# Optimization experiments

Hardware: AMD Instinct MI355X
Metric: run time of the kernel (lower is better)

Reference implementation:

```python
import jax, jax.numpy as jnp
import numpy as np
from jax import lax

B, L, V = 128, 64, 8192
E = H = 128
STEPS = 10
MAX_BIN = 512
BETA_START, BETA_END = 1e-4, 2e-2


def setup_inputs():
    key = jax.random.key(0)
    k = jax.random.split(key, 23)
    s = 0.05
    padded_x = (jax.random.uniform(k[0], (B, L, V)) < 0.01).astype(jnp.float32)
    lengths = jax.random.randint(k[1], (B,), 1, L + 1)
    visit_mask = (jnp.arange(L)[None, :] < lengths[:, None]).astype(jnp.float32)
    padded_bins = jnp.sort(jax.random.randint(k[2], (B, L), 0, MAX_BIN), axis=1)
    t_diff = jax.random.randint(k[3], (B,), 1, STEPS + 1)
    eps = jax.random.normal(k[4], (B, L, E))
    z0 = jax.random.normal(k[5], (B, L, E))
    noise = jax.random.normal(k[6], (STEPS, B, L, E))
    W_visit = jax.random.normal(k[7], (E, V)) * s
    bin_embed = (jax.random.normal(k[8], (MAX_BIN + 2, E)) * s).at[0].set(0.0)  # padding_idx=0
    W_ih = jax.random.normal(k[9], (4 * H, E)) * s
    W_hh = jax.random.normal(k[10], (4 * H, H)) * s
    b_ih = jax.random.normal(k[11], (4 * H,)) * s
    b_hh = jax.random.normal(k[12], (4 * H,)) * s
    W_cls = jax.random.normal(k[13], (1, H)) * s
    b_cls = jax.random.normal(k[14], (1,)) * s
    W_proj = jax.random.normal(k[15], (E, H)) * s
    time_embed = jax.random.normal(k[16], (STEPS + 1, E)) * s
    W_fuse = jax.random.normal(k[17], (2, 2 * E)) * s
    b_fuse = jax.random.normal(k[18], (2,)) * s
    W_e1 = jax.random.normal(k[19], (E, 2 * E)) * s
    b_e1 = jax.random.normal(k[20], (E,)) * s
    W_e2 = jax.random.normal(k[21], (E, E)) * s
    b_e2 = jax.random.normal(k[22], (E,)) * s
    return dict(padded_x=padded_x, visit_mask=visit_mask, padded_bins=padded_bins,
                t_diff=t_diff, eps=eps, z0=z0, noise=noise, W_visit=W_visit,
                bin_embed=bin_embed, W_ih=W_ih, W_hh=W_hh, b_ih=b_ih, b_hh=b_hh,
                W_cls=W_cls, b_cls=b_cls, W_proj=W_proj, time_embed=time_embed,
                W_fuse=W_fuse, b_fuse=b_fuse, W_e1=W_e1, b_e1=b_e1, W_e2=W_e2, b_e2=b_e2)


def _lstm(v, W_ih, W_hh, b_ih, b_hh):
    # v: [B,L,E] -> h: [B,L,H]; PyTorch gate order i,f,g,o
    xg = jnp.einsum('ble,ge->blg', v, W_ih) + b_ih + b_hh
    def step(carry, x):
        h, c = carry
        g = x + h @ W_hh.T
        i, f, gg, o = jnp.split(g, 4, axis=-1)
        c = jax.nn.sigmoid(f) * c + jax.nn.sigmoid(i) * jnp.tanh(gg)
        h = jax.nn.sigmoid(o) * jnp.tanh(c)
        return (h, c), h
    z = jnp.zeros((v.shape[0], W_hh.shape[1]), v.dtype)
    _, hs = lax.scan(step, (z, z), jnp.swapaxes(xg, 0, 1))
    return jnp.swapaxes(hs, 0, 1)


def _last_hidden(h, mask):
    lengths = jnp.maximum(mask.sum(axis=1).astype(jnp.int32), 1)
    return h[jnp.arange(h.shape[0]), lengths - 1]


def reference(padded_x, visit_mask, padded_bins, t_diff, eps, z0, noise,
              W_visit, bin_embed, W_ih, W_hh, b_ih, b_hh, W_cls, b_cls,
              W_proj, time_embed, W_fuse, b_fuse, W_e1, b_e1, W_e2, b_e2):
    m = visit_mask[..., None]                      # [B,L,1]
    betas = jnp.linspace(BETA_START, BETA_END, STEPS)
    alphas = 1.0 - betas
    alpha_bars = jnp.cumprod(alphas)

    # visit embedding + time-gap (delta bin) embedding
    delta = jnp.concatenate([jnp.zeros_like(padded_bins[:, :1]),
                             jnp.clip(padded_bins[:, 1:] - padded_bins[:, :-1], 0)], axis=1)
    delta = jnp.where(visit_mask > 0, jnp.clip(delta, 0, MAX_BIN + 1), 0)
    v = (padded_x @ W_visit.T + bin_embed[delta]) * m  # [B,L,E]

    # encoder LSTM (packed seq == plain scan then zero padded suffix positions)
    h = _lstm(v, W_ih, W_hh, b_ih, b_hh) * m
    logits_real = (_last_hidden(h, visit_mask) @ W_cls.T + b_cls)[:, 0]

    h_prev = jnp.pad(h[:, :-1], ((0, 0), (1, 0), (0, 0)))
    hp = (h_prev @ W_proj.T) * m                   # [B,L,E]

    def fuse_eps(z, t_emb):
        a = jax.nn.softmax(jnp.concatenate([z, hp], -1) @ W_fuse.T + b_fuse, axis=-1)
        g = a[..., :1] * z + a[..., 1:] * hp
        x = jnp.concatenate([g, t_emb], -1)
        return jax.nn.relu(x @ W_e1.T + b_e1) @ W_e2.T + b_e2

    # diffusion loss
    t = jnp.where(visit_mask > 0, t_diff[:, None], 1)    # [B,L]
    ab = alpha_bars[t - 1][..., None]
    z_t = (jnp.sqrt(ab) * v + jnp.sqrt(1.0 - ab) * eps) * m
    eps_pred = fuse_eps(z_t, time_embed[t])
    denom = jnp.maximum(visit_mask.sum(), 1.0)
    diffusion_loss = jnp.sum((eps_pred - eps) ** 2 * m) / denom

    # reverse diffusion sampling of synthetic visit embeddings
    def step(z, inp):
        kk, nz = inp
        t_s = jnp.where(visit_mask > 0, kk, 1)
        e = fuse_eps(z, time_embed[t_s])
        beta = betas[kk - 1]
        mean = (z - beta / jnp.sqrt(1.0 - alpha_bars[kk - 1]) * e) / jnp.sqrt(alphas[kk - 1])
        z = jnp.where(kk > 1, mean + jnp.sqrt(beta) * nz, mean) * m
        return z, None

    ks = jnp.arange(STEPS, 0, -1)
    v_syn, _ = lax.scan(step, z0, (ks, noise))

    h_syn = _lstm(v_syn, W_ih, W_hh, b_ih, b_hh) * m
    logits_syn = (_last_hidden(h_syn, visit_mask) @ W_cls.T + b_cls)[:, 0]
    return logits_real, logits_syn, diffusion_loss
```

## Files before the change

### kernel.cpp

```cpp
#include <hip/hip_runtime.h>

#define B_ 128
#define L_ 64
#define V_ 8192
#define E_ 128
#define H_ 128
#define NROW (B_*L_)
#define HSTRIDE 136
#define AS 136
#define XS 264
#define YS 136
#define ZS 132

typedef unsigned short u16;
typedef __attribute__((ext_vector_type(8))) short bf16x8;
typedef __attribute__((ext_vector_type(4))) float f32x4;

__device__ __forceinline__ float sigm(float x){ return 1.f/(1.f + __expf(-x)); }
__device__ __forceinline__ float ftanh(float x){ float e = __expf(2.f*x); return 1.f - 2.f/(e + 1.f); }
__device__ __forceinline__ u16 f2bf(float f){
    union { unsigned int i; float f; } x; x.f = f;
    unsigned int r = x.i + 0x7fff + ((x.i >> 16) & 1);
    return (u16)(r >> 16);
}
#define LBAR() asm volatile("s_waitcnt lgkmcnt(0)\ns_barrier" ::: "memory")

__device__ __forceinline__ bf16x8 pack8(const float* p){
    const float4* q = (const float4*)p;
    float4 a = q[0], b = q[1];
    bf16x8 f;
    f[0]=(short)f2bf(a.x); f[1]=(short)f2bf(a.y); f[2]=(short)f2bf(a.z); f[3]=(short)f2bf(a.w);
    f[4]=(short)f2bf(b.x); f[5]=(short)f2bf(b.y); f[6]=(short)f2bf(b.z); f[7]=(short)f2bf(b.w);
    return f;
}

__global__ __launch_bounds__(256) void k_transpose_wv(const float* __restrict__ Wv, float* __restrict__ WT){
    __shared__ float tile[16][129];
    int v0 = blockIdx.x * 16;
    int t = threadIdx.x;
    #pragma unroll
    for(int i=0;i<8;i++){
        int idx = i*256 + t; int e = idx >> 4; int vv = idx & 15;
        tile[vv][e] = Wv[(size_t)e*V_ + v0 + vv];
    }
    __syncthreads();
    #pragma unroll
    for(int i=0;i<8;i++){
        int idx = i*256 + t; int vv = idx >> 7; int e = idx & 127;
        WT[(size_t)(v0+vv)*E_ + e] = tile[vv][e];
    }
}

__global__ __launch_bounds__(256) void k_visit_embed(const float* __restrict__ px, const float* __restrict__ vmask,
                                                     const int* __restrict__ bins, const float* __restrict__ bemb,
                                                     const float* __restrict__ WT, float* __restrict__ v){
    __shared__ int idxs[512];
    __shared__ int cnt;
    __shared__ int dsh;
    __shared__ float msh;
    __shared__ float4 red[8][32];
    int row = blockIdx.x; int l = row & 63;
    int t = threadIdx.x;
    if(t==0){
        cnt = 0;
        float m = vmask[row];
        int d = 0;
        if(l > 0){ d = bins[row] - bins[row-1]; d = d < 0 ? 0 : (d > 513 ? 513 : d); }
        if(!(m > 0.f)) d = 0;
        dsh = d; msh = m;
    }
    __syncthreads();
    const uint4* xr4 = (const uint4*)(px + (size_t)row * V_);
    for(int i=t;i<2048;i+=256){
        uint4 u = xr4[i];
        unsigned int w[4] = {u.x,u.y,u.z,u.w};
        #pragma unroll
        for(int j=0;j<4;j++){
            if(w[j]){ int p = atomicAdd(&cnt,1); if(p<512) idxs[p] = i*4 + j; }
        }
    }
    __syncthreads();
    int n = cnt; if(n > 512) n = 512;
    int eq = t & 31, jg = t >> 5;
    float4 a4 = {0.f,0.f,0.f,0.f};
    for(int j=jg;j<n;j+=8){
        const float4* wr = (const float4*)(WT + (size_t)idxs[j]*E_);
        float4 wv = wr[eq];
        a4.x += wv.x; a4.y += wv.y; a4.z += wv.z; a4.w += wv.w;
    }
    red[jg][eq] = a4;
    __syncthreads();
    if(t < 32){
        float4 s = red[0][t];
        #pragma unroll
        for(int g=1;g<8;g++){
            float4 r = red[g][t];
            s.x += r.x; s.y += r.y; s.z += r.z; s.w += r.w;
        }
        const float4* bp = (const float4*)(bemb + dsh*E_);
        float4 bv = bp[t];
        float m = msh;
        float4 o;
        o.x = (s.x + bv.x)*m; o.y = (s.y + bv.y)*m; o.z = (s.z + bv.z)*m; o.w = (s.w + bv.w)*m;
        ((float4*)(v + (size_t)row*E_))[t] = o;
    }
}

template<bool DOHP>
__device__ __forceinline__ void lstm_step(int l,
        const u16* __restrict__ bufr, u16* __restrict__ bufw,
        const u16* __restrict__ vbr, u16* __restrict__ vbw,
        const float*& pv, float*& hpb,
        const bf16x8 (&bfh)[4][4], const bf16x8 (&bfv)[4][4], const bf16x8 (&wp)[4],
        const float (&bb)[4], float (&c4)[4], float (&lg4)[4], const int (&len4)[4],
        float wcv, int t, int lc, int quad, int cw){
    float4 vnx;
    if(l+1 < 64){ vnx = *(const float4*)pv; pv += E_; }
    bf16x8 afh[4], afv[4];
    #pragma unroll
    for(int kt=0;kt<4;kt++){
        afh[kt] = *(const bf16x8*)&bufr[lc*HSTRIDE + kt*32 + quad*8];
        afv[kt] = *(const bf16x8*)&vbr[lc*AS + kt*32 + quad*8];
    }
    f32x4 acc[4], acch;
    #pragma unroll
    for(int g=0;g<4;g++) acc[g] = (f32x4){0.f,0.f,0.f,0.f};
    acch = (f32x4){0.f,0.f,0.f,0.f};
    #pragma unroll
    for(int kt=0;kt<4;kt++){
        #pragma unroll
        for(int g=0;g<4;g++){
            acc[g] = __builtin_amdgcn_mfma_f32_16x16x32_bf16(afh[kt], bfh[g][kt], acc[g], 0,0,0);
            acc[g] = __builtin_amdgcn_mfma_f32_16x16x32_bf16(afv[kt], bfv[g][kt], acc[g], 0,0,0);
        }
        if constexpr (DOHP)
            acch = __builtin_amdgcn_mfma_f32_16x16x32_bf16(afh[kt], wp[kt], acch, 0,0,0);
    }
    if constexpr (DOHP){
        #pragma unroll
        for(int r=0;r<4;r++) hpb[(size_t)r*64*E_] = acch[r];
        hpb += E_;
    }
    #pragma unroll
    for(int r=0;r<4;r++){
        float gi = acc[0][r] + bb[0];
        float gf = acc[1][r] + bb[1];
        float gg = acc[2][r] + bb[2];
        float go = acc[3][r] + bb[3];
        float c  = sigm(gf)*c4[r] + sigm(gi)*ftanh(gg);
        float h  = sigm(go)*ftanh(c);
        c4[r] = c;
        bufw[(quad*4+r)*HSTRIDE + cw] = f2bf(h);
        if(l == len4[r]-1) lg4[r] += h * wcv;
    }
    if(l+1 < 64){
        int sr = t >> 5, se = (t & 31)*4;
        u16* d = vbw + sr*AS + se;
        d[0]=f2bf(vnx.x); d[1]=f2bf(vnx.y); d[2]=f2bf(vnx.z); d[3]=f2bf(vnx.w);
    }
    LBAR();
}

template<bool DOHP>
__global__ __launch_bounds__(512,1) void k_lstm_fused(const float* __restrict__ vin,
        const float* __restrict__ Whh, const float* __restrict__ Wih,
        const float* __restrict__ bih, const float* __restrict__ bhh,
        const float* __restrict__ Wproj, const float* __restrict__ Wcls, const float* __restrict__ bcls,
        const float* __restrict__ vmask, float* __restrict__ hp_out, float* __restrict__ logits_out){
    __shared__ __align__(16) u16 hbuf[2][16*HSTRIDE];
    __shared__ __align__(16) u16 vbuf[2][16*AS];
    __shared__ float vmsh[16*64];
    __shared__ int lensh[16];
    __shared__ float lgsh[16][132];
    int t = threadIdx.x;
    int wave = t >> 6, lane = t & 63;
    int quad = lane >> 4, lc = lane & 15;
    int cw = wave*16 + lc;
    int b0 = blockIdx.x * 16;

    for(int i=t;i<16*HSTRIDE;i+=512) hbuf[0][i] = 0;
    for(int i=t;i<1024;i+=512) vmsh[i] = vmask[b0*64 + i];
    const float* pv = vin + (size_t)(b0 + (t>>5))*64*E_ + (t&31)*4;
    {
        float4 v0 = *(const float4*)pv; pv += E_;
        u16* d = &vbuf[0][(t>>5)*AS + (t&31)*4];
        d[0]=f2bf(v0.x); d[1]=f2bf(v0.y); d[2]=f2bf(v0.z); d[3]=f2bf(v0.w);
    }
    __syncthreads();
    if(t < 16){
        int s = 0;
        #pragma unroll
        for(int i=0;i<64;i++) s += (vmsh[t*64 + i] > 0.f) ? 1 : 0;
        lensh[t] = s < 1 ? 1 : s;
    }

    bf16x8 bfh[4][4], bfv[4][4], wp[4];
    float bb[4];
    #pragma unroll
    for(int g=0;g<4;g++){
        int n = g*128 + cw;
        bb[g] = bih[n] + bhh[n];
        const float* wrh = Whh + (size_t)n*H_ + quad*8;
        const float* wrv = Wih + (size_t)n*E_ + quad*8;
        #pragma unroll
        for(int kt=0;kt<4;kt++){ bfh[g][kt] = pack8(wrh + kt*32); bfv[g][kt] = pack8(wrv + kt*32); }
    }
    if constexpr (DOHP){
        const float* wr = Wproj + (size_t)cw*H_ + quad*8;
        #pragma unroll
        for(int kt=0;kt<4;kt++) wp[kt] = pack8(wr + kt*32);
    }
    float wcv = Wcls[cw];
    float c4[4] = {0.f,0.f,0.f,0.f};
    float lg4[4] = {0.f,0.f,0.f,0.f};
    float* hpb = DOHP ? (hp_out + (size_t)(b0 + quad*4)*64*E_ + cw) : nullptr;
    __syncthreads();
    int len4[4];
    #pragma unroll
    for(int r=0;r<4;r++) len4[r] = lensh[quad*4 + r];

    for(int lb=0;lb<64;lb+=2){
        lstm_step<DOHP>(lb,   hbuf[0], hbuf[1], vbuf[0], vbuf[1], pv, hpb, bfh, bfv, wp, bb, c4, lg4, len4, wcv, t, lc, quad, cw);
        lstm_step<DOHP>(lb+1, hbuf[1], hbuf[0], vbuf[1], vbuf[0], pv, hpb, bfh, bfv, wp, bb, c4, lg4, len4, wcv, t, lc, quad, cw);
    }
    #pragma unroll
    for(int r=0;r<4;r++) lgsh[quad*4+r][cw] = lg4[r];
    __syncthreads();
    {
        int row = t >> 5, l32 = t & 31;
        float s = lgsh[row][l32] + lgsh[row][l32+32] + lgsh[row][l32+64] + lgsh[row][l32+96];
        s += __shfl_down(s, 16, 32);
        s += __shfl_down(s, 8, 32);
        s += __shfl_down(s, 4, 32);
        s += __shfl_down(s, 2, 32);
        s += __shfl_down(s, 1, 32);
        if(l32 == 0) logits_out[b0 + row] = s + bcls[0];
    }
}

__global__ __launch_bounds__(256,2) void k_drg(const float* __restrict__ v, const float* __restrict__ hp,
        const float* __restrict__ eps, const int* __restrict__ tdiff, const float* __restrict__ vmask,
        const float* __restrict__ z0, const float* __restrict__ noise, const float* __restrict__ temb,
        const float* __restrict__ Wf, const float* __restrict__ bfu,
        const float* __restrict__ We1, const float* __restrict__ be1,
        const float* __restrict__ We2, const float* __restrict__ be2,
        float* __restrict__ partial, float* __restrict__ vsyn){
    __shared__ __align__(16) float zbuf[16*ZS];
    __shared__ float hpbuf[16*ZS];
    __shared__ __align__(16) u16 xbuf[16*XS];
    __shared__ __align__(16) u16 y1buf[16*YS];
    __shared__ float wfsh[512];
    __shared__ float ssh[16][2], hpd[16][2];
    __shared__ float mrow[16]; __shared__ int trow[16];
    __shared__ float sbeta[10], sabar[10];
    __shared__ float rb[4];
    int row0 = blockIdx.x * 16; int t = threadIdx.x;
    int wave = t >> 6, lane = t & 63, quad = lane >> 4, lc = lane & 15;

    if(t==0){
        float p = 1.f;
        for(int k=0;k<10;k++){ float b = 1e-4f + (0.02f - 1e-4f)*k/9.f; sbeta[k] = b; p *= (1.f - b); sabar[k] = p; }
    }
    if(t < 16){
        int row = row0 + t; float m = vmask[row];
        mrow[t] = m; trow[t] = (m > 0.f) ? tdiff[row >> 6] : 1;
    }
    for(int i=t;i<512;i+=256) wfsh[i] = Wf[i];
    __syncthreads();
    #pragma unroll
    for(int i=0;i<8;i++){
        int flat = i*256 + t; int r = flat >> 7; int e = flat & 127; int row = row0 + r;
        float ab = sabar[trow[r]-1];
        zbuf[r*ZS + e] = (sqrtf(ab)*v[(size_t)row*E_ + e] + sqrtf(1.f - ab)*eps[(size_t)row*E_ + e]) * mrow[r];
        hpbuf[r*ZS + e] = hp[(size_t)row*E_ + e];
    }
    bf16x8 wf1[2][8], wf2[2][4];
    float be1v[2], be2v[2];
    #pragma unroll
    for(int nt=0;nt<2;nt++){
        int n = wave*32 + nt*16 + lc;
        be1v[nt] = be1[n]; be2v[nt] = be2[n];
        const float* w1 = We1 + (size_t)n*256 + quad*8;
        #pragma unroll
        for(int kt=0;kt<8;kt++) wf1[nt][kt] = pack8(w1 + kt*32);
        const float* w2 = We2 + (size_t)n*128 + quad*8;
        #pragma unroll
        for(int kt=0;kt<4;kt++) wf2[nt][kt] = pack8(w2 + kt*32);
    }
    __syncthreads();
    {
        int row = t >> 4, k = (t >> 3) & 1, sub = t & 7;
        float p = 0.f;
        #pragma unroll
        for(int i=0;i<16;i++)
            p += hpbuf[row*ZS + sub*16 + i] * wfsh[k*256 + 128 + sub*16 + i];
        p += __shfl_down(p,4); p += __shfl_down(p,2); p += __shfl_down(p,1);
        if(sub == 0) hpd[row][k] = p + bfu[k];
    }
    __syncthreads();

    for(int s=0;s<11;s++){
        int kk = 11 - s;
        float nzv[8], epv[8], z0v[8];
        if(s >= 1){
            #pragma unroll
            for(int nt=0;nt<2;nt++)
                #pragma unroll
                for(int r=0;r<4;r++)
                    nzv[nt*4+r] = noise[((size_t)(s-1)*NROW + row0 + quad*4 + r)*E_ + wave*32 + nt*16 + lc];
        } else {
            #pragma unroll
            for(int nt=0;nt<2;nt++)
                #pragma unroll
                for(int r=0;r<4;r++)
                    epv[nt*4+r] = eps[(size_t)(row0 + quad*4 + r)*E_ + wave*32 + nt*16 + lc];
            #pragma unroll
            for(int i=0;i<8;i++){
                int flat = i*256 + t;
                z0v[i] = z0[(size_t)(row0 + (flat >> 7))*E_ + (flat & 127)];
            }
        }
        {
            int row = t >> 4, k = (t >> 3) & 1, sub = t & 7;
            float q = 0.f;
            #pragma unroll
            for(int i=0;i<16;i++)
                q += zbuf[row*ZS + sub*16 + i] * wfsh[k*256 + sub*16 + i];
            q += __shfl_down(q,4); q += __shfl_down(q,2); q += __shfl_down(q,1);
            if(sub == 0) ssh[row][k] = q + hpd[row][k];
        }
        __syncthreads();
        {
            int row = t >> 4, c0 = (t & 15) * 16;
            float s0 = ssh[row][0], s1 = ssh[row][1];
            float a0 = 1.f/(1.f + __expf(s1 - s0)), a1 = 1.f - a0;
            int tt = (s == 0) ? trow[row] : ((mrow[row] > 0.f) ? kk : 1);
            #pragma unroll
            for(int i=0;i<16;i++){
                int c = c0 + i;
                float val = (c < 128) ? (a0*zbuf[row*ZS + c] + a1*hpbuf[row*ZS + c])
                                      : temb[tt*E_ + (c - 128)];
                xbuf[row*XS + c] = f2bf(val);
            }
        }
        __syncthreads();
        f32x4 acc1[2];
        acc1[0] = (f32x4){0.f,0.f,0.f,0.f}; acc1[1] = (f32x4){0.f,0.f,0.f,0.f};
        #pragma unroll
        for(int kt=0;kt<8;kt++){
            bf16x8 af = *(const bf16x8*)&xbuf[lc*XS + kt*32 + quad*8];
            acc1[0] = __builtin_amdgcn_mfma_f32_16x16x32_bf16(af, wf1[0][kt], acc1[0], 0,0,0);
            acc1[1] = __builtin_amdgcn_mfma_f32_16x16x32_bf16(af, wf1[1][kt], acc1[1], 0,0,0);
        }
        #pragma unroll
        for(int nt=0;nt<2;nt++){
            #pragma unroll
            for(int r=0;r<4;r++)
                y1buf[(quad*4+r)*YS + wave*32 + nt*16 + lc] = f2bf(fmaxf(acc1[nt][r] + be1v[nt], 0.f));
        }
        __syncthreads();
        f32x4 acc2[2];
        acc2[0] = (f32x4){0.f,0.f,0.f,0.f}; acc2[1] = (f32x4){0.f,0.f,0.f,0.f};
        #pragma unroll
        for(int kt=0;kt<4;kt++){
            bf16x8 af = *(const bf16x8*)&y1buf[lc*YS + kt*32 + quad*8];
            acc2[0] = __builtin_amdgcn_mfma_f32_16x16x32_bf16(af, wf2[0][kt], acc2[0], 0,0,0);
            acc2[1] = __builtin_amdgcn_mfma_f32_16x16x32_bf16(af, wf2[1][kt], acc2[1], 0,0,0);
        }
        if(s == 0){
            float lp = 0.f;
            #pragma unroll
            for(int nt=0;nt<2;nt++){
                #pragma unroll
                for(int r=0;r<4;r++){
                    int m = quad*4 + r;
                    float d = (acc2[nt][r] + be2v[nt]) - epv[nt*4+r];
                    lp += d*d*mrow[m];
                }
            }
            #pragma unroll
            for(int off=32;off;off>>=1) lp += __shfl_down(lp, off);
            if(lane == 0) rb[wave] = lp;
            __syncthreads();
            if(t == 0) partial[blockIdx.x] = rb[0]+rb[1]+rb[2]+rb[3];
            #pragma unroll
            for(int i=0;i<8;i++){
                int flat = i*256 + t; int r = flat >> 7; int e = flat & 127;
                zbuf[r*ZS + e] = z0v[i];
            }
            __syncthreads();
        } else {
            float beta = sbeta[kk-1];
            float c1 = beta / sqrtf(1.f - sabar[kk-1]);
            float c2 = 1.f / sqrtf(1.f - beta);
            float sb = sqrtf(beta);
            #pragma unroll
            for(int nt=0;nt<2;nt++){
                int n = wave*32 + nt*16 + lc;
                #pragma unroll
                for(int r=0;r<4;r++){
                    int m = quad*4 + r;
                    float e = acc2[nt][r] + be2v[nt];
                    float z = zbuf[m*ZS + n];
                    float mean = (z - c1*e) * c2;
                    float nz = nzv[nt*4+r];
                    float znew = (kk > 1) ? (mean + sb*nz) : mean;
                    zbuf[m*ZS + n] = znew * mrow[m];
                }
            }
            __syncthreads();
        }
    }
    {
        int r = t >> 4, e0 = (t & 15) * 8;
        float4 a = *(const float4*)&zbuf[r*ZS + e0];
        float4 b2 = *(const float4*)&zbuf[r*ZS + e0 + 4];
        *(float4*)&vsyn[(size_t)(row0 + r)*E_ + e0] = a;
        *(float4*)&vsyn[(size_t)(row0 + r)*E_ + e0 + 4] = b2;
    }
}

__global__ void k_finalize(const float* __restrict__ partial, const float* __restrict__ vmask, float* __restrict__ out){
    __shared__ float rb[4], rl[4];
    int t = threadIdx.x;
    float s = 0.f;
    for(int i=t;i<NROW;i+=256) s += vmask[i];
    float ls = 0.f;
    for(int i=t;i<512;i+=256) ls += partial[i];
    #pragma unroll
    for(int off=32;off;off>>=1){ s += __shfl_down(s, off); ls += __shfl_down(ls, off); }
    if((t & 63) == 0){ rb[t >> 6] = s; rl[t >> 6] = ls; }
    __syncthreads();
    if(t == 0){
        float denom = rb[0]+rb[1]+rb[2]+rb[3];
        if(denom < 1.f) denom = 1.f;
        out[256] = (rl[0]+rl[1]+rl[2]+rl[3]) / denom;
    }
}

extern "C" void kernel_launch(void* const* d_in, const int* in_sizes, int n_in,
                              void* d_out, int out_size, void* d_ws, size_t ws_size,
                              hipStream_t stream){
    const float* px    = (const float*)d_in[0];
    const float* vmask = (const float*)d_in[1];
    const int*   bins  = (const int*)d_in[2];
    const int*   tdiff = (const int*)d_in[3];
    const float* eps   = (const float*)d_in[4];
    const float* z0    = (const float*)d_in[5];
    const float* noise = (const float*)d_in[6];
    const float* Wv    = (const float*)d_in[7];
    const float* bemb  = (const float*)d_in[8];
    const float* Wih   = (const float*)d_in[9];
    const float* Whh   = (const float*)d_in[10];
    const float* bih   = (const float*)d_in[11];
    const float* bhh   = (const float*)d_in[12];
    const float* Wcls  = (const float*)d_in[13];
    const float* bcls  = (const float*)d_in[14];
    const float* Wproj = (const float*)d_in[15];
    const float* temb  = (const float*)d_in[16];
    const float* Wf    = (const float*)d_in[17];
    const float* bfu   = (const float*)d_in[18];
    const float* We1   = (const float*)d_in[19];
    const float* be1   = (const float*)d_in[20];
    const float* We2   = (const float*)d_in[21];
    const float* be2   = (const float*)d_in[22];
    float* out = (float*)d_out;

    float* ws      = (float*)d_ws;
    float* WT      = ws;
    float* v       = ws + 1048576;
    float* vsyn    = ws + 2097152;
    float* hp      = ws + 3145728;
    float* partial = ws + 4194304;

    hipLaunchKernelGGL(k_transpose_wv, dim3(V_/16), dim3(256), 0, stream, Wv, WT);
    hipLaunchKernelGGL(k_visit_embed, dim3(NROW), dim3(256), 0, stream, px, vmask, bins, bemb, WT, v);
    hipLaunchKernelGGL((k_lstm_fused<true>), dim3(B_/16), dim3(512), 0, stream,
                       v, Whh, Wih, bih, bhh, Wproj, Wcls, bcls, vmask, hp, out);
    hipLaunchKernelGGL(k_drg, dim3(NROW/16), dim3(256), 0, stream,
                       v, hp, eps, tdiff, vmask, z0, noise, temb, Wf, bfu,
                       We1, be1, We2, be2, partial, vsyn);
    hipLaunchKernelGGL((k_lstm_fused<false>), dim3(B_/16), dim3(512), 0, stream,
                       vsyn, Whh, Wih, bih, bhh, Wproj, Wcls, bcls, vmask, (float*)nullptr, out + 128);
    hipLaunchKernelGGL(k_finalize, dim3(1), dim3(256), 0, stream, partial, vmask, out);
}
```

Baseline: 819.9 us.

## Hoist LSTM input projection into parallel GEMM and prepack weights to bf16

Moves the input-to-gate projection (v @ W_ih) out of the sequential LSTM recurrence into a separate, fully parallel MFMA GEMM kernel. The recurrent kernel then only does the h @ W_hh MFMAs and streams precomputed gate preactivations from global memory. A pack kernel converts the weights once into MFMA-fragment bf16 layout. The W_proj projection moves out of the LSTM into k_drg, computed from stored bf16 hidden states. This shortens the serial critical path, but adds extra kernels and a large fp32 gate buffer that is written and then read back.

```diff
diff --git a/kernel.cpp b/kernel.cpp
--- a/kernel.cpp
+++ b/kernel.cpp
@@ -11,6 +11,7 @@
 #define XS 264
 #define YS 136
 #define ZS 132
+#define HS2 136
 
 typedef unsigned short u16;
 typedef __attribute__((ext_vector_type(8))) short bf16x8;
@@ -106,69 +107,119 @@
     }
 }
 
-template<bool DOHP>
+__global__ __launch_bounds__(256) void k_pack(const float* __restrict__ Whh, const float* __restrict__ Wih,
+                                              const float* __restrict__ We1, const float* __restrict__ We2,
+                                              const float* __restrict__ Wproj,
+                                              u16* __restrict__ dWhh, u16* __restrict__ dWih,
+                                              u16* __restrict__ dWe1, u16* __restrict__ dWe2,
+                                              u16* __restrict__ dWproj){
+    int bid = blockIdx.x; int t = threadIdx.x;
+    const float* src; u16* dst; int WS,TS,NT,KT,K; int base;
+    if(bid<32){ src=Whh; dst=dWhh; WS=16; TS=128; NT=4; KT=4; K=128; base=bid; }
+    else if(bid<64){ src=Wih; dst=dWih; WS=128; TS=16; NT=8; KT=4; K=128; base=bid-32; }
+    else if(bid<80){ src=We1; dst=dWe1; WS=32; TS=16; NT=2; KT=8; K=256; base=bid-64; }
+    else if(bid<88){ src=We2; dst=dWe2; WS=32; TS=16; NT=2; KT=4; K=128; base=bid-80; }
+    else { src=Wproj; dst=dWproj; WS=32; TS=16; NT=2; KT=4; K=128; base=bid-88; }
+    for(int i=0;i<8;i++){
+        int o = base*2048 + i*256 + t;
+        int g = o >> 9; int lane = (o >> 3) & 63; int j = o & 7;
+        int kt = g % KT; int r2 = g / KT; int nt = r2 % NT; int w = r2 / NT;
+        int lc = lane & 15; int quad = lane >> 4;
+        int n = w*WS + nt*TS + lc; int k = kt*32 + quad*8 + j;
+        dst[o] = f2bf(src[(size_t)n*K + k]);
+    }
+}
+
+__global__ __launch_bounds__(256,2) void k_gemm_xgp(const float* __restrict__ A, const u16* __restrict__ Wihp,
+                                                    const float* __restrict__ bih, const float* __restrict__ bhh,
+                                                    float* __restrict__ xgp){
+    __shared__ __align__(16) u16 abuf[16*AS];
+    int t = threadIdx.x, wave = t >> 6, lane = t & 63, quad = lane >> 4, lc = lane & 15;
+    int bid = blockIdx.x; int bg = bid >> 6, l = bid & 63;
+    #pragma unroll
+    for(int i=0;i<8;i++){
+        int flat = i*256 + t; int r = flat >> 7, e = flat & 127;
+        abuf[r*AS + e] = f2bf(A[((size_t)(bg*16+r)*64 + l)*E_ + e]);
+    }
+    bf16x8 wg[8][4]; float bb[8];
+    #pragma unroll
+    for(int nt=0;nt<8;nt++){
+        int n = wave*128 + nt*16 + lc;
+        bb[nt] = bih[n] + bhh[n];
+        #pragma unroll
+        for(int kt=0;kt<4;kt++)
+            wg[nt][kt] = *(const bf16x8*)(Wihp + (((wave*8+nt)*4+kt)<<9) + lane*8);
+    }
+    __syncthreads();
+    f32x4 ac[8];
+    #pragma unroll
+    for(int nt=0;nt<8;nt++) ac[nt] = (f32x4){0.f,0.f,0.f,0.f};
+    #pragma unroll
+    for(int kt=0;kt<4;kt++){
+        bf16x8 af = *(const bf16x8*)&abuf[lc*AS + kt*32 + quad*8];
+        #pragma unroll
+        for(int nt=0;nt<8;nt++)
+            ac[nt] = __builtin_amdgcn_mfma_f32_16x16x32_bf16(af, wg[nt][kt], ac[nt], 0,0,0);
+    }
+    float* dst = xgp + (size_t)bid*8192;
+    #pragma unroll
+    for(int nt=0;nt<8;nt++){
+        float4 o;
+        o.x = ac[nt][0] + bb[nt]; o.y = ac[nt][1] + bb[nt];
+        o.z = ac[nt][2] + bb[nt]; o.w = ac[nt][3] + bb[nt];
+        *(float4*)(dst + nt*1024 + quad*256 + lc*16 + wave*4) = o;
+    }
+}
+
+template<bool STOREH>
 __device__ __forceinline__ void lstm_step(int l,
         const u16* __restrict__ bufr, u16* __restrict__ bufw,
-        const u16* __restrict__ vbr, u16* __restrict__ vbw,
-        const float*& pv, float*& hpb,
-        const bf16x8 (&bfh)[4][4], const bf16x8 (&bfv)[4][4], const bf16x8 (&wp)[4],
-        const float (&bb)[4], float (&c4)[4], float (&lg4)[4], const int (&len4)[4],
-        float wcv, int t, int lc, int quad, int cw){
-    float4 vnx;
-    if(l+1 < 64){ vnx = *(const float4*)pv; pv += E_; }
-    bf16x8 afh[4], afv[4];
+        const f32x4*& pxg, u16* hsp,
+        const bf16x8 (&bfh)[4][4],
+        f32x4 (&xc)[4], f32x4 (&xn)[4], float (&c4)[4], float (&lg4)[4],
+        const int (&len4)[4], float wcv, int lc, int quad, int cw){
+    if(l+1 < 64){
+        #pragma unroll
+        for(int g=0;g<4;g++) xn[g] = pxg[g];
+        pxg += 2048;
+    }
+    bf16x8 afh[4];
+    #pragma unroll
+    for(int kt=0;kt<4;kt++)
+        afh[kt] = *(const bf16x8*)&bufr[lc*HSTRIDE + kt*32 + quad*8];
+    f32x4 acc[4];
+    #pragma unroll
+    for(int g=0;g<4;g++) acc[g] = (f32x4){0.f,0.f,0.f,0.f};
     #pragma unroll
     for(int kt=0;kt<4;kt++){
-        afh[kt] = *(const bf16x8*)&bufr[lc*HSTRIDE + kt*32 + quad*8];
-        afv[kt] = *(const bf16x8*)&vbr[lc*AS + kt*32 + quad*8];
-    }
-    f32x4 acc[4], acch;
-    #pragma unroll
-    for(int g=0;g<4;g++) acc[g] = (f32x4){0.f,0.f,0.f,0.f};
-    acch = (f32x4){0.f,0.f,0.f,0.f};
-    #pragma unroll
-    for(int kt=0;kt<4;kt++){
-        #pragma unroll
-        for(int g=0;g<4;g++){
+        #pragma unroll
+        for(int g=0;g<4;g++)
             acc[g] = __builtin_amdgcn_mfma_f32_16x16x32_bf16(afh[kt], bfh[g][kt], acc[g], 0,0,0);
-            acc[g] = __builtin_amdgcn_mfma_f32_16x16x32_bf16(afv[kt], bfv[g][kt], acc[g], 0,0,0);
-        }
-        if constexpr (DOHP)
-            acch = __builtin_amdgcn_mfma_f32_16x16x32_bf16(afh[kt], wp[kt], acch, 0,0,0);
-    }
-    if constexpr (DOHP){
-        #pragma unroll
-        for(int r=0;r<4;r++) hpb[(size_t)r*64*E_] = acch[r];
-        hpb += E_;
     }
     #pragma unroll
     for(int r=0;r<4;r++){
-        float gi = acc[0][r] + bb[0];
-        float gf = acc[1][r] + bb[1];
-        float gg = acc[2][r] + bb[2];
-        float go = acc[3][r] + bb[3];
+        float gi = acc[0][r] + xc[0][r];
+        float gf = acc[1][r] + xc[1][r];
+        float gg = acc[2][r] + xc[2][r];
+        float go = acc[3][r] + xc[3][r];
         float c  = sigm(gf)*c4[r] + sigm(gi)*ftanh(gg);
         float h  = sigm(go)*ftanh(c);
         c4[r] = c;
-        bufw[(quad*4+r)*HSTRIDE + cw] = f2bf(h);
+        u16 hb = f2bf(h);
+        bufw[(quad*4+r)*HSTRIDE + cw] = hb;
+        if constexpr (STOREH) hsp[(size_t)r*8192 + (size_t)l*128] = hb;
         if(l == len4[r]-1) lg4[r] += h * wcv;
     }
-    if(l+1 < 64){
-        int sr = t >> 5, se = (t & 31)*4;
-        u16* d = vbw + sr*AS + se;
-        d[0]=f2bf(vnx.x); d[1]=f2bf(vnx.y); d[2]=f2bf(vnx.z); d[3]=f2bf(vnx.w);
-    }
     LBAR();
 }
 
-template<bool DOHP>
-__global__ __launch_bounds__(512,1) void k_lstm_fused(const float* __restrict__ vin,
-        const float* __restrict__ Whh, const float* __restrict__ Wih,
-        const float* __restrict__ bih, const float* __restrict__ bhh,
-        const float* __restrict__ Wproj, const float* __restrict__ Wcls, const float* __restrict__ bcls,
-        const float* __restrict__ vmask, float* __restrict__ hp_out, float* __restrict__ logits_out){
+template<bool STOREH>
+__global__ __attribute__((amdgpu_waves_per_eu(2,2))) __launch_bounds__(512)
+void k_lstm(const float* __restrict__ xgp, const u16* __restrict__ Whhp,
+            const float* __restrict__ Wcls, const float* __restrict__ bcls,
+            const float* __restrict__ vmask, u16* __restrict__ h_store,
+            float* __restrict__ logits_out){
     __shared__ __align__(16) u16 hbuf[2][16*HSTRIDE];
-    __shared__ __align__(16) u16 vbuf[2][16*AS];
     __shared__ float vmsh[16*64];
     __shared__ int lensh[16];
     __shared__ float lgsh[16][132];
@@ -176,16 +227,10 @@
     int wave = t >> 6, lane = t & 63;
     int quad = lane >> 4, lc = lane & 15;
     int cw = wave*16 + lc;
-    int b0 = blockIdx.x * 16;
+    int bg = blockIdx.x; int b0 = bg * 16;
 
     for(int i=t;i<16*HSTRIDE;i+=512) hbuf[0][i] = 0;
     for(int i=t;i<1024;i+=512) vmsh[i] = vmask[b0*64 + i];
-    const float* pv = vin + (size_t)(b0 + (t>>5))*64*E_ + (t&31)*4;
-    {
-        float4 v0 = *(const float4*)pv; pv += E_;
-        u16* d = &vbuf[0][(t>>5)*AS + (t&31)*4];
-        d[0]=f2bf(v0.x); d[1]=f2bf(v0.y); d[2]=f2bf(v0.z); d[3]=f2bf(v0.w);
-    }
     __syncthreads();
     if(t < 16){
         int s = 0;
@@ -194,34 +239,30 @@
         lensh[t] = s < 1 ? 1 : s;
     }
 
-    bf16x8 bfh[4][4], bfv[4][4], wp[4];
-    float bb[4];
-    #pragma unroll
-    for(int g=0;g<4;g++){
-        int n = g*128 + cw;
-        bb[g] = bih[n] + bhh[n];
-        const float* wrh = Whh + (size_t)n*H_ + quad*8;
-        const float* wrv = Wih + (size_t)n*E_ + quad*8;
-        #pragma unroll
-        for(int kt=0;kt<4;kt++){ bfh[g][kt] = pack8(wrh + kt*32); bfv[g][kt] = pack8(wrv + kt*32); }
-    }
-    if constexpr (DOHP){
-        const float* wr = Wproj + (size_t)cw*H_ + quad*8;
-        #pragma unroll
-        for(int kt=0;kt<4;kt++) wp[kt] = pack8(wr + kt*32);
-    }
+    bf16x8 bfh[4][4];
+    #pragma unroll
+    for(int g=0;g<4;g++)
+        #pragma unroll
+        for(int kt=0;kt<4;kt++)
+            bfh[g][kt] = *(const bf16x8*)(Whhp + (((wave*4+g)*4+kt)<<9) + lane*8);
     float wcv = Wcls[cw];
     float c4[4] = {0.f,0.f,0.f,0.f};
     float lg4[4] = {0.f,0.f,0.f,0.f};
-    float* hpb = DOHP ? (hp_out + (size_t)(b0 + quad*4)*64*E_ + cw) : nullptr;
+    u16* hsp = STOREH ? (h_store + ((size_t)(b0 + quad*4)*64)*128 + cw) : (u16*)nullptr;
+
+    const f32x4* pxg = (const f32x4*)(xgp + (size_t)bg*64*8192) + t*4;
+    f32x4 x0[4], x1[4];
+    #pragma unroll
+    for(int g=0;g<4;g++) x0[g] = pxg[g];
+    pxg += 2048;
     __syncthreads();
     int len4[4];
     #pragma unroll
     for(int r=0;r<4;r++) len4[r] = lensh[quad*4 + r];
 
     for(int lb=0;lb<64;lb+=2){
-        lstm_step<DOHP>(lb,   hbuf[0], hbuf[1], vbuf[0], vbuf[1], pv, hpb, bfh, bfv, wp, bb, c4, lg4, len4, wcv, t, lc, quad, cw);
-        lstm_step<DOHP>(lb+1, hbuf[1], hbuf[0], vbuf[1], vbuf[0], pv, hpb, bfh, bfv, wp, bb, c4, lg4, len4, wcv, t, lc, quad, cw);
+        lstm_step<STOREH>(lb,   hbuf[0], hbuf[1], pxg, hsp, bfh, x0, x1, c4, lg4, len4, wcv, lc, quad, cw);
+        lstm_step<STOREH>(lb+1, hbuf[1], hbuf[0], pxg, hsp, bfh, x1, x0, c4, lg4, len4, wcv, lc, quad, cw);
     }
     #pragma unroll
     for(int r=0;r<4;r++) lgsh[quad*4+r][cw] = lg4[r];
@@ -238,17 +279,19 @@
     }
 }
 
-__global__ __launch_bounds__(256,2) void k_drg(const float* __restrict__ v, const float* __restrict__ hp,
+__global__ __launch_bounds__(256,2) void k_drg(const float* __restrict__ v, const u16* __restrict__ h,
         const float* __restrict__ eps, const int* __restrict__ tdiff, const float* __restrict__ vmask,
         const float* __restrict__ z0, const float* __restrict__ noise, const float* __restrict__ temb,
         const float* __restrict__ Wf, const float* __restrict__ bfu,
-        const float* __restrict__ We1, const float* __restrict__ be1,
-        const float* __restrict__ We2, const float* __restrict__ be2,
+        const u16* __restrict__ We1p, const float* __restrict__ be1,
+        const u16* __restrict__ We2p, const float* __restrict__ be2,
+        const u16* __restrict__ Wprojp,
         float* __restrict__ partial, float* __restrict__ vsyn){
     __shared__ __align__(16) float zbuf[16*ZS];
     __shared__ float hpbuf[16*ZS];
     __shared__ __align__(16) u16 xbuf[16*XS];
     __shared__ __align__(16) u16 y1buf[16*YS];
+    __shared__ __align__(16) u16 hb16[16*HS2];
     __shared__ float wfsh[512];
     __shared__ float ssh[16][2], hpd[16][2];
     __shared__ float mrow[16]; __shared__ int trow[16];
@@ -272,20 +315,46 @@
         int flat = i*256 + t; int r = flat >> 7; int e = flat & 127; int row = row0 + r;
         float ab = sabar[trow[r]-1];
         zbuf[r*ZS + e] = (sqrtf(ab)*v[(size_t)row*E_ + e] + sqrtf(1.f - ab)*eps[(size_t)row*E_ + e]) * mrow[r];
-        hpbuf[r*ZS + e] = hp[(size_t)row*E_ + e];
-    }
-    bf16x8 wf1[2][8], wf2[2][4];
+    }
+    {
+        int r = t >> 4, e0 = (t & 15) * 8;
+        bf16x8 hv;
+        if(((row0 & 63) == 0) && r == 0){
+            hv = (bf16x8){0,0,0,0,0,0,0,0};
+        } else {
+            hv = *(const bf16x8*)(h + (size_t)(row0 - 1 + r)*E_ + e0);
+        }
+        *(bf16x8*)&hb16[r*HS2 + e0] = hv;
+    }
+    bf16x8 wf1[2][8], wf2[2][4], pf[2][4];
     float be1v[2], be2v[2];
     #pragma unroll
     for(int nt=0;nt<2;nt++){
         int n = wave*32 + nt*16 + lc;
         be1v[nt] = be1[n]; be2v[nt] = be2[n];
-        const float* w1 = We1 + (size_t)n*256 + quad*8;
-        #pragma unroll
-        for(int kt=0;kt<8;kt++) wf1[nt][kt] = pack8(w1 + kt*32);
-        const float* w2 = We2 + (size_t)n*128 + quad*8;
-        #pragma unroll
-        for(int kt=0;kt<4;kt++) wf2[nt][kt] = pack8(w2 + kt*32);
+        #pragma unroll
+        for(int kt=0;kt<8;kt++) wf1[nt][kt] = *(const bf16x8*)(We1p + (((wave*2+nt)*8+kt)<<9) + lane*8);
+        #pragma unroll
+        for(int kt=0;kt<4;kt++){
+            wf2[nt][kt] = *(const bf16x8*)(We2p + (((wave*2+nt)*4+kt)<<9) + lane*8);
+            pf[nt][kt]  = *(const bf16x8*)(Wprojp + (((wave*2+nt)*4+kt)<<9) + lane*8);
+        }
+    }
+    __syncthreads();
+    {
+        f32x4 ap[2];
+        ap[0] = (f32x4){0.f,0.f,0.f,0.f}; ap[1] = (f32x4){0.f,0.f,0.f,0.f};
+        #pragma unroll
+        for(int kt=0;kt<4;kt++){
+            bf16x8 af = *(const bf16x8*)&hb16[lc*HS2 + kt*32 + quad*8];
+            ap[0] = __builtin_amdgcn_mfma_f32_16x16x32_bf16(af, pf[0][kt], ap[0], 0,0,0);
+            ap[1] = __builtin_amdgcn_mfma_f32_16x16x32_bf16(af, pf[1][kt], ap[1], 0,0,0);
+        }
+        #pragma unroll
+        for(int nt=0;nt<2;nt++)
+            #pragma unroll
+            for(int rr=0;rr<4;rr++)
+                hpbuf[(quad*4+rr)*ZS + wave*32 + nt*16 + lc] = ap[nt][rr];
     }
     __syncthreads();
     {
@@ -466,21 +535,31 @@
     const float* be2   = (const float*)d_in[22];
     float* out = (float*)d_out;
 
-    float* ws      = (float*)d_ws;
-    float* WT      = ws;
-    float* v       = ws + 1048576;
-    float* vsyn    = ws + 2097152;
-    float* hp      = ws + 3145728;
-    float* partial = ws + 4194304;
+    float* ws = (float*)d_ws;
+    float* xgp     = ws;
+    float* WT      = ws + 4194304;
+    u16*  Whh_p    = (u16*)(ws + 4194304);
+    u16*  Wih_p    = (u16*)(ws + 4227072);
+    u16*  We1_p    = (u16*)(ws + 4259840);
+    u16*  We2_p    = (u16*)(ws + 4276224);
+    u16*  Wproj_p  = (u16*)(ws + 4284416);
+    u16*  h_store  = (u16*)(ws + 4292608);
+    float* v       = ws + 5242880;
+    float* vsyn    = ws + 6291456;
+    float* partial = ws + 7340032;
 
     hipLaunchKernelGGL(k_transpose_wv, dim3(V_/16), dim3(256), 0, stream, Wv, WT);
     hipLaunchKernelGGL(k_visit_embed, dim3(NROW), dim3(256), 0, stream, px, vmask, bins, bemb, WT, v);
-    hipLaunchKernelGGL((k_lstm_fused<true>), dim3(B_/16), dim3(512), 0, stream,
-                       v, Whh, Wih, bih, bhh, Wproj, Wcls, bcls, vmask, hp, out);
+    hipLaunchKernelGGL(k_pack, dim3(96), dim3(256), 0, stream, Whh, Wih, We1, We2, Wproj,
+                       Whh_p, Wih_p, We1_p, We2_p, Wproj_p);
+    hipLaunchKernelGGL(k_gemm_xgp, dim3(512), dim3(256), 0, stream, v, Wih_p, bih, bhh, xgp);
+    hipLaunchKernelGGL((k_lstm<true>), dim3(B_/16), dim3(512), 0, stream,
+                       xgp, Whh_p, Wcls, bcls, vmask, h_store, out);
     hipLaunchKernelGGL(k_drg, dim3(NROW/16), dim3(256), 0, stream,
-                       v, hp, eps, tdiff, vmask, z0, noise, temb, Wf, bfu,
-                       We1, be1, We2, be2, partial, vsyn);
-    hipLaunchKernelGGL((k_lstm_fused<false>), dim3(B_/16), dim3(512), 0, stream,
-                       vsyn, Whh, Wih, bih, bhh, Wproj, Wcls, bcls, vmask, (float*)nullptr, out + 128);
+                       v, h_store, eps, tdiff, vmask, z0, noise, temb, Wf, bfu,
+                       We1_p, be1, We2_p, be2, Wproj_p, partial, vsyn);
+    hipLaunchKernelGGL(k_gemm_xgp, dim3(512), dim3(256), 0, stream, vsyn, Wih_p, bih, bhh, xgp);
+    hipLaunchKernelGGL((k_lstm<false>), dim3(B_/16), dim3(512), 0, stream,
+                       xgp, Whh_p, Wcls, bcls, vmask, (u16*)nullptr, out + 128);
     hipLaunchKernelGGL(k_finalize, dim3(1), dim3(256), 0, stream, partial, vmask, out);
 }
```

Result: faster. 742.3 us (-9.5%).
